# Kernel tuning notes

Measured on AMD Instinct MI355X. Metric: run time of the kernel, lower is better.

The kernel has to match this reference:

```python
import jax, jax.numpy as jnp
import numpy as np
from jax import lax

B, T, V = 128, 256, 64
HF = 32   # MLP feature-imputation hidden
CTX = 32  # context hidden
HID = 64  # LSTM hidden


def _uniform(k, shape, fan):
    s = 1.0 / np.sqrt(fan)
    return jax.random.uniform(k, shape, jnp.float32, -s, s)


def setup_inputs():
    key = jax.random.key(0)
    ks = jax.random.split(key, 40)
    values = jax.random.normal(ks[0], (B, T, V), jnp.float32)
    masks = (jax.random.uniform(ks[1], (B, T, V)) > 0.3).astype(jnp.float32)
    deltas = jax.random.uniform(ks[2], (B, T, V), jnp.float32) * 5.0
    lengths = jax.random.randint(ks[3], (B,), T // 2, T + 1)
    min_vals = jnp.min(values, axis=1, keepdims=True)
    max_vals = jnp.max(values, axis=1, keepdims=True)
    D_in = 2 * V + 2 * CTX
    return dict(
        lengths=lengths, values=values, masks=masks, deltas=deltas,
        min_vals=min_vals, max_vals=max_vals,
        W_decay=_uniform(ks[4], (V, V), V), b_decay=_uniform(ks[5], (V,), V),
        W_feat=_uniform(ks[6], (V, HF, V), V), b_feat=_uniform(ks[7], (V, HF), V),
        W_nl1=_uniform(ks[8], (HF, HF), HF), b_nl1=_uniform(ks[9], (HF,), HF),
        W_nl2=_uniform(ks[10], (1, HF), HF), b_nl2=_uniform(ks[11], (1,), HF),
        Wc1=_uniform(ks[12], (2 * CTX, 3 * V + 1), 3 * V + 1), bc1=_uniform(ks[13], (2 * CTX,), 3 * V + 1),
        Wc2=_uniform(ks[14], (CTX, 2 * CTX), 2 * CTX), bc2=_uniform(ks[15], (CTX,), 2 * CTX),
        W_ih_g=_uniform(ks[16], (3 * CTX, 2 * V), CTX), W_hh_g=_uniform(ks[17], (3 * CTX, CTX), CTX),
        b_ih_g=_uniform(ks[18], (3 * CTX,), CTX), b_hh_g=_uniform(ks[19], (3 * CTX,), CTX),
        W_init=_uniform(ks[20], (2 * HID, 2 * CTX), 2 * CTX), b_init=_uniform(ks[21], (2 * HID,), 2 * CTX),
        W_ih_f=_uniform(ks[22], (4 * HID, D_in), HID), W_hh_f=_uniform(ks[23], (4 * HID, HID), HID),
        b_ih_f=_uniform(ks[24], (4 * HID,), HID), b_hh_f=_uniform(ks[25], (4 * HID,), HID),
        W_ih_b=_uniform(ks[26], (4 * HID, D_in), HID), W_hh_b=_uniform(ks[27], (4 * HID, HID), HID),
        b_ih_b=_uniform(ks[28], (4 * HID,), HID), b_hh_b=_uniform(ks[29], (4 * HID,), HID),
        W_ri=_uniform(ks[30], (V, 2 * HID), 2 * HID), b_ri=_uniform(ks[31], (V,), 2 * HID),
        W_fu=_uniform(ks[32], (V, 2 * V), 2 * V), b_fu=_uniform(ks[33], (V,), 2 * V),
    )


def _gru(x, h, Wih, Whh, bih, bhh):
    gi = x @ Wih.T + bih
    gh = h @ Whh.T + bhh
    ir, iz, inn = jnp.split(gi, 3, axis=-1)
    hr, hz, hn = jnp.split(gh, 3, axis=-1)
    r = jax.nn.sigmoid(ir + hr)
    z = jax.nn.sigmoid(iz + hz)
    n = jnp.tanh(inn + r * hn)
    return (1.0 - z) * n + z * h


def _lstm(x, h, c, Wih, Whh, bih, bhh):
    g = x @ Wih.T + bih + h @ Whh.T + bhh
    i, f, gg, o = jnp.split(g, 4, axis=-1)
    c = jax.nn.sigmoid(f) * c + jax.nn.sigmoid(i) * jnp.tanh(gg)
    h = jax.nn.sigmoid(o) * jnp.tanh(c)
    return h, c


def _forward(lengths, values, masks, deltas, min_vals, max_vals,
             W_decay, b_decay, W_feat, b_feat, W_nl1, b_nl1, W_nl2, b_nl2,
             Wc1, bc1, Wc2, bc2, W_ih_g, W_hh_g, b_ih_g, b_hh_g,
             W_init, b_init, W_ih_f, W_hh_f, b_ih_f, b_hh_f,
             W_ih_b, W_hh_b, b_ih_b, b_hh_b, W_ri, b_ri, W_fu, b_fu):
    Bb, Tt, Vv = values.shape
    lf = lengths.astype(jnp.float32)
    pad = (jnp.arange(Tt)[None, :] + 1 <= lengths[:, None]).astype(jnp.float32)  # [B,T]

    msum = masks.sum(axis=1)                       # [B,V] observation counts
    means = values.sum(axis=1) / msum
    var = ((values - means[:, None, :]) ** 2).sum(axis=1) / (msum - 1.0)
    stdev = jnp.sqrt(var)
    missing = 1.0 - msum / lf[:, None]
    stats = jnp.concatenate([lf[:, None], means, stdev, missing], axis=1)  # [B,3V+1]

    mmn = jnp.maximum(max_vals - min_vals, 1e-8)   # [B,1,V]
    nv = (values - min_vals) / mmn
    nmeans = (means - min_vals[:, 0, :]) / mmn[:, 0, :]

    # last-observation-carried-forward x_prime
    nv_tm = jnp.swapaxes(nv, 0, 1)   # [T,B,V]
    m_tm = jnp.swapaxes(masks, 0, 1)

    def pstep(xp, xm):
        x_prev, m_prev = xm
        xp = m_prev * x_prev + (1.0 - m_prev) * xp
        return xp, xp
    _, xp_rest = lax.scan(pstep, nv_tm[0], (nv_tm[:-1], m_tm[:-1]))
    x_prime = jnp.swapaxes(jnp.concatenate([nv_tm[:1], xp_rest], axis=0), 0, 1)

    # InputTemporalDecay: F.linear(d, W*I, b) == d * diag(W) + b
    gamma = jnp.exp(-jax.nn.relu(deltas * jnp.diag(W_decay) + b_decay))
    x_decay = gamma * x_prime + (1.0 - gamma) * nmeans[:, None, :]
    x_complete = masks * nv + (1.0 - masks) * x_decay

    # context vectors
    ctx_mlp = jax.nn.relu(stats @ Wc1.T + bc1) @ Wc2.T + bc2  # [B,CTX]
    x_rnn_tm = jnp.swapaxes(jnp.concatenate([x_complete, masks], axis=-1), 0, 1)  # [T,B,2V]
    pad_tm = jnp.swapaxes(pad, 0, 1)[:, :, None]
    h0 = jnp.zeros((Bb, W_hh_g.shape[1]), values.dtype)

    def gstep(carry, inp):
        h, hn = carry
        x_t, p_t = inp
        h = _gru(x_t, h, W_ih_g, W_hh_g, b_ih_g, b_hh_g)
        hn = p_t * h + (1.0 - p_t) * hn
        return (h, hn), None
    (_, ctx_rnn), _ = lax.scan(gstep, (h0, h0), (x_rnn_tm, pad_tm))
    context = jnp.concatenate([ctx_mlp, ctx_rnn], axis=1)  # [B,2*CTX]

    hinit = context @ W_init.T + b_init  # [B,2H]
    cinit = jnp.tanh(hinit)
    Hh = hinit.shape[1] // 2
    hf0, hb0 = hinit[:, :Hh], hinit[:, Hh:]
    cf0, cb0 = cinit[:, :Hh], cinit[:, Hh:]

    ctx_bt = jnp.broadcast_to(context[:, None, :], (Bb, Tt, context.shape[1]))
    rnn_in_tm = jnp.swapaxes(jnp.concatenate([x_complete, masks, ctx_bt], axis=-1), 0, 1)  # [T,B,D]

    def fstep(carry, x):
        h, c = _lstm(x, carry[0], carry[1], W_ih_f, W_hh_f, b_ih_f, b_hh_f)
        return (h, c), h
    _, hf_rest = lax.scan(fstep, (hf0, cf0), rnn_in_tm[:-1])
    hf_all = jnp.concatenate([hf0[None], hf_rest], axis=0)  # [T,B,H]

    def bstep(carry, x):
        h, c = _lstm(x, carry[0], carry[1], W_ih_b, W_hh_b, b_ih_b, b_hh_b)
        return (h, c), h
    _, hb_rest = lax.scan(bstep, (hb0, cb0), rnn_in_tm[1:][::-1])  # t = T-1 .. 1
    hb_all = jnp.concatenate([hb0[None], hb_rest], axis=0)[::-1]   # time-aligned

    h_cat = jnp.concatenate([hf_all, hb_all], axis=-1)  # [T,B,2H]
    rnn_imp = jnp.swapaxes(h_cat @ W_ri.T + b_ri, 0, 1)  # [B,T,V]

    # per-variable masked feature imputation (no self-connection)
    eye = jnp.eye(Vv, dtype=values.dtype)
    Wm = W_feat * (1.0 - eye[:, None, :])                 # [V,HF,V]
    hidden = jnp.einsum('btv,ghv->btgh', x_complete, Wm) + b_feat  # [B,T,V,HF]
    z = jax.nn.relu(hidden) @ W_nl1.T + b_nl1
    feat_imp = (jax.nn.relu(z) @ W_nl2.T + b_nl2)[..., 0]  # [B,T,V]

    beta = jax.nn.sigmoid(jnp.concatenate([gamma, masks], axis=-1) @ W_fu.T + b_fu)
    final_imp = beta * feat_imp + (1.0 - beta) * rnn_imp

    # unnormalize all three estimates; stack as [3,B,T,V]
    out = jnp.stack([rnn_imp, feat_imp, final_imp], axis=0) * mmn[None] + min_vals[None]
    return out


def reference(lengths, values, masks, deltas, min_vals, max_vals,
              W_decay, b_decay, W_feat, b_feat, W_nl1, b_nl1, W_nl2, b_nl2,
              Wc1, bc1, Wc2, bc2, W_ih_g, W_hh_g, b_ih_g, b_hh_g,
              W_init, b_init, W_ih_f, W_hh_f, b_ih_f, b_hh_f,
              W_ih_b, W_hh_b, b_ih_b, b_hh_b, W_ri, b_ri, W_fu, b_fu):
    return _forward(lengths, values, masks, deltas, min_vals, max_vals,
                    W_decay, b_decay, W_feat, b_feat, W_nl1, b_nl1, W_nl2, b_nl2,
                    Wc1, bc1, Wc2, bc2, W_ih_g, W_hh_g, b_ih_g, b_hh_g,
                    W_init, b_init, W_ih_f, W_hh_f, b_ih_f, b_hh_f,
                    W_ih_b, W_hh_b, b_ih_b, b_hh_b, W_ri, b_ri, W_fu, b_fu)
```

## Files before the change

### kernel.cpp

```cpp
#include <hip/hip_runtime.h>
#include <hip/hip_fp16.h>

static constexpr int NB = 128;
static constexpr int NT = 256;
static constexpr int NV = 64;
static constexpr int NBT = NB * NT;
static constexpr int NBTV = NBT * NV;

typedef __attribute__((ext_vector_type(8))) short short8;
typedef __attribute__((ext_vector_type(4))) float f32x4;
typedef __attribute__((ext_vector_type(4))) float fvec4;

__device__ __forceinline__ void wave_lds_fence() {
    __builtin_amdgcn_sched_barrier(0);
    asm volatile("s_waitcnt lgkmcnt(0)" ::: "memory");
    __builtin_amdgcn_sched_barrier(0);
}

__device__ __forceinline__ void block_sync_lds() {
    __builtin_amdgcn_sched_barrier(0);
    asm volatile("s_waitcnt lgkmcnt(0)" ::: "memory");
    __builtin_amdgcn_s_barrier();
    asm volatile("" ::: "memory");
    __builtin_amdgcn_sched_barrier(0);
}

__device__ __forceinline__ unsigned short f2bf(float x) {
    unsigned int u = __float_as_uint(x);
    return (unsigned short)((u + 0x7FFFu + ((u >> 16) & 1u)) >> 16);
}
__device__ __forceinline__ float bf2f(unsigned short b) {
    return __uint_as_float(((unsigned int)b) << 16);
}
__device__ __forceinline__ unsigned short f2h(float x) {
    union { _Float16 h; unsigned short u; } c; c.h = (_Float16)x; return c.u;
}
__device__ __forceinline__ float fsigm(float x) {
    return __builtin_amdgcn_rcpf(1.0f + __expf(-x));
}
__device__ __forceinline__ float ftanh(float x) {
    return 1.0f - 2.0f * __builtin_amdgcn_rcpf(1.0f + __expf(2.0f * x));
}

__device__ __forceinline__ short8 pack8(float4 a, float4 b) {
    short8 r;
    r[0] = (short)f2bf(a.x); r[1] = (short)f2bf(a.y); r[2] = (short)f2bf(a.z); r[3] = (short)f2bf(a.w);
    r[4] = (short)f2bf(b.x); r[5] = (short)f2bf(b.y); r[6] = (short)f2bf(b.z); r[7] = (short)f2bf(b.w);
    return r;
}

__device__ __forceinline__ void dot4(float4& acc, const float4 wv, const float4 xv) {
    acc.x = fmaf(wv.x, xv.x, acc.x);
    acc.y = fmaf(wv.y, xv.y, acc.y);
    acc.z = fmaf(wv.z, xv.z, acc.z);
    acc.w = fmaf(wv.w, xv.w, acc.w);
}

__global__ __launch_bounds__(256) void k_prep(
    const float* __restrict__ Wf, const float* __restrict__ Wihf,
    const float* __restrict__ Wihb, const float* __restrict__ Wihg,
    const float* __restrict__ Whhf, const float* __restrict__ Whhb,
    const float* __restrict__ Whhg, const float* __restrict__ Wri,
    const float* __restrict__ Wfu,
    unsigned short* __restrict__ wbf, float* __restrict__ wdiag,
    unsigned short* __restrict__ wgf, unsigned short* __restrict__ wgb,
    unsigned short* __restrict__ wgg,
    unsigned short* __restrict__ whhf_h, unsigned short* __restrict__ whhb_h,
    unsigned short* __restrict__ whhg_h,
    unsigned short* __restrict__ wri_bf, unsigned short* __restrict__ wfu_bf) {
    int i = blockIdx.x * 256 + threadIdx.x;
    if (i < NV * 32 * NV) wbf[i] = f2bf(Wf[i]);
    if (i < 2048) wdiag[i] = bf2f(f2bf(Wf[i * 64 + (i >> 5)]));
    if (i < 32768) {
        int n = i >> 7, k = i & 127;
        wgf[i] = f2bf(Wihf[n * 192 + k]);
        wgb[i] = f2bf(Wihb[n * 192 + k]);
    }
    if (i < 12288) wgg[i] = f2bf(Wihg[i]);
    if (i < 16384) { whhf_h[i] = f2h(Whhf[i]); whhb_h[i] = f2h(Whhb[i]); }
    if (i < 3072) whhg_h[i] = f2h(Whhg[i]);
    if (i < 8192) { wri_bf[i] = f2bf(Wri[i]); wfu_bf[i] = f2bf(Wfu[i]); }
}

__global__ __launch_bounds__(256) void k_fill(
    const int* __restrict__ lengths,
    const float* __restrict__ values, const float* __restrict__ masks,
    const float* __restrict__ deltas, const float* __restrict__ minv,
    const float* __restrict__ maxv,
    const float* __restrict__ Wd, const float* __restrict__ bd,
    float* __restrict__ stats,
    float* __restrict__ mmn_ws, float* __restrict__ nmeans_ws,
    float* __restrict__ xcomp, float* __restrict__ gam) {
    int b = blockIdx.x; int tid = threadIdx.x;
    int v = tid & 63; int tc = tid >> 6;
    float mn = minv[b * NV + v];
    size_t base = (size_t)b * NT * NV + v;
    __shared__ float red[3][4][64];
    __shared__ float lastv[4][64];
    __shared__ int hasf[4][64];
    __shared__ float nv0s[64];
    __shared__ float smm[64], snm[64];
    int t0 = tc * 64;
    float sv = 0.f, sq = 0.f, sm = 0.f;
    float last = 0.f; int has = 0;
    for (int t = t0; t < t0 + 64; t++) {
        float val = values[base + (size_t)t * NV];
        float m = masks[base + (size_t)t * NV];
        sv += val; sq += val * val; sm += m;
        if (m != 0.f) { last = val; has = 1; }
        if (tc == 0 && t == 0) nv0s[v] = val;
    }
    red[0][tc][v] = sv; red[1][tc][v] = sq; red[2][tc][v] = sm;
    lastv[tc][v] = last; hasf[tc][v] = has;
    __syncthreads();
    if (tc == 0) {
        sv = red[0][0][v] + red[0][1][v] + red[0][2][v] + red[0][3][v];
        sq = red[1][0][v] + red[1][1][v] + red[1][2][v] + red[1][3][v];
        sm = red[2][0][v] + red[2][1][v] + red[2][2][v] + red[2][3][v];
        float mean = sv / sm;
        float var = (sq - 2.0f * mean * sv + (float)NT * mean * mean) / (sm - 1.0f);
        var = fmaxf(var, 0.0f);
        float sd = sqrtf(var);
        float lf = (float)lengths[b];
        float miss = 1.0f - sm / lf;
        float mx = maxv[b * NV + v];
        float mm = fmaxf(mx - mn, 1e-8f);
        float* st = stats + b * 256;
        if (v == 0) st[0] = lf;
        st[1 + v] = mean; st[65 + v] = sd; st[129 + v] = miss;
        float nmean = (mean - mn) / mm;
        mmn_ws[b * NV + v] = mm;
        nmeans_ws[b * NV + v] = nmean;
        smm[v] = mm; snm[v] = nmean;
    }
    __syncthreads();
    float mm = smm[v];
    float nmean = snm[v];
    float wd = Wd[v * NV + v], bdv = bd[v];
    float xp = (nv0s[v] - mn) / mm;
    for (int q = tc - 1; q >= 0; q--) {
        if (hasf[q][v]) { xp = (lastv[q][v] - mn) / mm; break; }
    }
    for (int t = t0; t < t0 + 64; t++) {
        size_t i = base + (size_t)t * NV;
        float val = values[i], m = masks[i], d = deltas[i];
        float nv = (val - mn) / mm;
        float g = expf(-fmaxf(fmaf(d, wd, bdv), 0.0f));
        float xd = g * xp + (1.0f - g) * nmean;
        float xc = m * nv + (1.0f - m) * xd;
        xcomp[i] = xc; gam[i] = g;
        xp = (m != 0.f) ? nv : xp;
    }
}

__global__ __launch_bounds__(256) void k_gates_g(
    const float* __restrict__ xcomp, const float* __restrict__ masks,
    const unsigned short* __restrict__ wgg, const float* __restrict__ bihg,
    float* __restrict__ gg) {
    int wave = threadIdx.x >> 6, lane = threadIdx.x & 63;
    int bt0 = blockIdx.x * 64 + wave * 16;
    int r = lane & 15, kc = lane >> 4;
    const float* xr = xcomp + (size_t)(bt0 + r) * NV + kc * 8;
    const float* mr = masks + (size_t)(bt0 + r) * NV + kc * 8;
    short8 af0 = pack8(*(const float4*)(xr), *(const float4*)(xr + 4));
    short8 af1 = pack8(*(const float4*)(xr + 32), *(const float4*)(xr + 36));
    short8 af2 = pack8(*(const float4*)(mr), *(const float4*)(mr + 4));
    short8 af3 = pack8(*(const float4*)(mr + 32), *(const float4*)(mr + 36));
    #pragma unroll 3
    for (int nt = 0; nt < 6; nt++) {
        const unsigned short* w = wgg + (size_t)(nt * 16 + r) * 128 + kc * 8;
        float bias = bihg[nt * 16 + r];
        f32x4 acc = {bias, bias, bias, bias};
        acc = __builtin_amdgcn_mfma_f32_16x16x32_bf16(af0, *(const short8*)(w), acc, 0, 0, 0);
        acc = __builtin_amdgcn_mfma_f32_16x16x32_bf16(af1, *(const short8*)(w + 32), acc, 0, 0, 0);
        acc = __builtin_amdgcn_mfma_f32_16x16x32_bf16(af2, *(const short8*)(w + 64), acc, 0, 0, 0);
        acc = __builtin_amdgcn_mfma_f32_16x16x32_bf16(af3, *(const short8*)(w + 96), acc, 0, 0, 0);
        #pragma unroll
        for (int i = 0; i < 4; i++)
            gg[(size_t)(bt0 + kc * 4 + i) * 96 + nt * 16 + r] = acc[i];
    }
}

#define GRU_STEP(T, GIN) { \
    const int t_ = (T); const int p_ = t_ & 1; \
    int4 raw_[4]; \
    const int4* hp_ = (const int4*)hsg[g][s]; \
    _Pragma("unroll") for (int q = 0; q < 4; q++) raw_[q] = hp_[q]; \
    const __half2* hhv_ = (const __half2*)raw_; \
    __half2 a0_ = zh2, a1_ = zh2, a2_ = zh2, a3_ = zh2; \
    _Pragma("unroll") for (int q = 0; q < 16; q += 4) { \
        a0_ = __hfma2(w2[q],     hhv_[q],     a0_); \
        a1_ = __hfma2(w2[q + 1], hhv_[q + 1], a1_); \
        a2_ = __hfma2(w2[q + 2], hhv_[q + 2], a2_); \
        a3_ = __hfma2(w2[q + 3], hhv_[q + 3], a3_); } \
    __half2 sA_ = __hadd2(__hadd2(a0_, a1_), __hadd2(a2_, a3_)); \
    float d_ = __low2float(sA_) + __high2float(sA_); \
    if (g < 2) { \
        gexg[p_][s][n][g] = GIN + bh + d_; \
    } else { \
        gexg[p_][s][n][2] = bh + d_; \
        gexg[p_][s][n][3] = GIN; \
    } \
    block_sync_lds(); \
    float qx_ = gexg[p_][s][n][0], qy_ = gexg[p_][s][n][1]; \
    float qz_ = gexg[p_][s][n][2], qw_ = gexg[p_][s][n][3]; \
    float rr_ = fsigm(qx_); \
    float zz_ = fsigm(qy_); \
    float nn_ = ftanh(qw_ + rr_ * qz_); \
    float h_ = (1.f - zz_) * nn_ + zz_ * hprev; \
    hprev = h_; \
    if (t_ < len) hn = h_; \
    hsg[g][s][n] = f2h(h_); \
    wave_lds_fence(); \
}

#define FEAT_BODY(BT0) { \
    int bt0 = (BT0); \
    int r = lane & 15, kc = lane >> 4; \
    unsigned short* hbw = hbs[wave]; \
    float* lx = ldsx[wave]; \
    float* flw = fls[wave]; \
    short8 a0, a1; \
    { \
        const float* xr = xcomp + (size_t)(bt0 + r) * NV + kc * 8; \
        a0 = pack8(*(const float4*)(xr), *(const float4*)(xr + 4)); \
        a1 = pack8(*(const float4*)(xr + 32), *(const float4*)(xr + 36)); \
    } \
    { \
        int gc0 = kc * 16; \
        const float* xr2 = xcomp + (size_t)(bt0 + r) * NV + gc0; \
        _Pragma("unroll") for (int e = 0; e < 16; e += 4) { \
            float4 p = *(const float4*)(xr2 + e); \
            lx[(gc0 + e + 0) * 16 + r] = bf2f(f2bf(p.x)); \
            lx[(gc0 + e + 1) * 16 + r] = bf2f(f2bf(p.y)); \
            lx[(gc0 + e + 2) * 16 + r] = bf2f(f2bf(p.z)); \
            lx[(gc0 + e + 3) * 16 + r] = bf2f(f2bf(p.w)); \
        } \
    } \
    short8 wb0, wb1; \
    { \
        const float* w = Wnl1 + r * 32 + kc * 8; \
        wb0 = pack8(*(const float4*)w, *(const float4*)(w + 4)); \
        const float* w2p = Wnl1 + (16 + r) * 32 + kc * 8; \
        wb1 = pack8(*(const float4*)w2p, *(const float4*)(w2p + 4)); \
    } \
    float b0i[4], b1i[4], w2a[4], w2b[4]; \
    _Pragma("unroll") for (int i = 0; i < 4; i++) { \
        b0i[i] = bnl1[kc * 4 + i]; \
        b1i[i] = bnl1[16 + kc * 4 + i]; \
        w2a[i] = Wnl2[kc * 4 + i]; \
        w2b[i] = Wnl2[16 + kc * 4 + i]; \
    } \
    float bn2 = bnl2[0]; \
    __builtin_amdgcn_wave_barrier(); \
    _Pragma("unroll 2") for (int g = 0; g < 64; g++) { \
        __builtin_amdgcn_wave_barrier(); \
        float xv[4]; \
        _Pragma("unroll") for (int i = 0; i < 4; i++) xv[i] = lx[g * 16 + kc * 4 + i]; \
        _Pragma("unroll") for (int f = 0; f < 2; f++) { \
            int n0 = g * 32 + f * 16; \
            const unsigned short* wrow = wbf + (size_t)(n0 + r) * 64; \
            short8 b0 = *(const short8*)(wrow + kc * 8); \
            short8 b1 = *(const short8*)(wrow + 32 + kc * 8); \
            f32x4 acc = {0.f, 0.f, 0.f, 0.f}; \
            acc = __builtin_amdgcn_mfma_f32_16x16x32_bf16(a0, b0, acc, 0, 0, 0); \
            acc = __builtin_amdgcn_mfma_f32_16x16x32_bf16(a1, b1, acc, 0, 0, 0); \
            int n = n0 + r; \
            float wd = wdiag[n], bs = bfeat[n]; \
            _Pragma("unroll") for (int i = 0; i < 4; i++) { \
                float h = acc[i] - xv[i] * wd + bs; \
                h = fmaxf(h, 0.0f); \
                hbw[(kc * 4 + i) * 32 + f * 16 + r] = f2bf(h); \
            } \
        } \
        __builtin_amdgcn_wave_barrier(); \
        short8 ah = *(const short8*)(hbw + r * 32 + kc * 8); \
        f32x4 zt0 = {0.f, 0.f, 0.f, 0.f}, zt1 = {0.f, 0.f, 0.f, 0.f}; \
        zt0 = __builtin_amdgcn_mfma_f32_16x16x32_bf16(wb0, ah, zt0, 0, 0, 0); \
        zt1 = __builtin_amdgcn_mfma_f32_16x16x32_bf16(wb1, ah, zt1, 0, 0, 0); \
        float p = 0.f; \
        _Pragma("unroll") for (int i = 0; i < 4; i++) { \
            p = fmaf(fmaxf(zt0[i] + b0i[i], 0.0f), w2a[i], p); \
            p = fmaf(fmaxf(zt1[i] + b1i[i], 0.0f), w2b[i], p); \
        } \
        p += __shfl_xor(p, 16, 64); \
        p += __shfl_xor(p, 32, 64); \
        if (lane < 16) flw[lane * 65 + g] = p + bn2; \
    } \
    __builtin_amdgcn_wave_barrier(); \
    _Pragma("unroll") for (int q = 0; q < 16; q++) \
        feat_out[(size_t)(bt0 + q) * NV + lane] = flw[q * 65 + lane]; \
}

__global__ __launch_bounds__(256, 1) void k_mid(
    const float* __restrict__ gg_t, const int* __restrict__ lengths,
    const unsigned short* __restrict__ whhg_h, const float* __restrict__ bhh,
    float* __restrict__ ctx,
    const float* __restrict__ stats, const float* __restrict__ Wc1,
    const float* __restrict__ bc1, const float* __restrict__ Wc2,
    const float* __restrict__ bc2,
    const float* __restrict__ xcomp, const float* __restrict__ masks,
    const unsigned short* __restrict__ wgf, const unsigned short* __restrict__ wgb,
    float* __restrict__ gf, float* __restrict__ gb) {
    __shared__ __align__(16) unsigned short hsg[3][2][32];
    __shared__ __align__(16) float gexg[2][2][32][5];
    __shared__ __align__(16) float ss[193];
    __shared__ float h1[64];

    int bx = blockIdx.x;
    int tid = threadIdx.x;

    if (bx < 64) {
        int b0 = bx * 2;
        int g = tid >> 6;
        int lane = tid & 63;
        int s = lane >> 5, n = lane & 31;
        if (g == 3) {
            for (int t = 0; t < NT; t++) block_sync_lds();
            return;
        }
        int b = b0 + s;
        const __half2 zh2 = __float2half2_rn(0.f);
        int4 w4[4];
        {
            const int4* wp = (const int4*)(whhg_h + (size_t)(g * 32 + n) * 32);
            #pragma unroll
            for (int q = 0; q < 4; q++) w4[q] = wp[q];
        }
        const __half2* w2 = (const __half2*)w4;
        float bh = bhh[g * 32 + n];
        int len = lengths[b];
        float hprev = 0.f, hn = 0.f;
        hsg[g][s][n] = f2h(0.f);
        const float* gbase = gg_t + (size_t)b * NT * 96;
        #define GGIDX(T) ((size_t)(T) * 96 + g * 32 + n)
        float gi0 = gbase[GGIDX(0)];
        float gi1 = gbase[GGIDX(1)];
        float gi2 = gbase[GGIDX(2)];
        float gi3 = gbase[GGIDX(3)];
        wave_lds_fence();
        for (int t = 0; t < 252; t += 4) {
            GRU_STEP(t, gi0)
            gi0 = gbase[GGIDX(t + 4)];
            GRU_STEP(t + 1, gi1)
            gi1 = gbase[GGIDX(t + 5)];
            GRU_STEP(t + 2, gi2)
            gi2 = gbase[GGIDX(t + 6)];
            GRU_STEP(t + 3, gi3)
            gi3 = gbase[GGIDX(t + 7)];
        }
        GRU_STEP(252, gi0)
        GRU_STEP(253, gi1)
        GRU_STEP(254, gi2)
        GRU_STEP(255, gi3)
        #undef GGIDX
        if (g == 0) ctx[(b0 + s) * 64 + 32 + n] = hn;
    } else if (bx < 192) {
        if (tid >= 64) return;
        int b = bx - 64;
        ss[tid] = stats[b * 256 + tid];
        ss[64 + tid] = stats[b * 256 + 64 + tid];
        ss[128 + tid] = stats[b * 256 + 128 + tid];
        if (tid == 0) ss[192] = stats[b * 256 + 192];
        wave_lds_fence();
        float acc = bc1[tid];
        const float* w = Wc1 + (size_t)tid * 193;
        for (int k = 0; k < 193; k++) acc = fmaf(w[k], ss[k], acc);
        h1[tid] = fmaxf(acc, 0.f);
        wave_lds_fence();
        if (tid < 32) {
            float a = bc2[tid];
            const float* w2 = Wc2 + tid * 64;
            for (int k = 0; k < 64; k++) a = fmaf(w2[k], h1[k], a);
            ctx[b * 64 + tid] = a;
        }
    } else {
        int wave = tid >> 6, lane = tid & 63;
        int bt0 = (bx - 192) * 64 + wave * 16;
        int r = lane & 15, kc = lane >> 4;
        const float* xr = xcomp + (size_t)(bt0 + r) * NV + kc * 8;
        const float* mr = masks + (size_t)(bt0 + r) * NV + kc * 8;
        short8 af0 = pack8(*(const float4*)(xr), *(const float4*)(xr + 4));
        short8 af1 = pack8(*(const float4*)(xr + 32), *(const float4*)(xr + 36));
        short8 af2 = pack8(*(const float4*)(mr), *(const float4*)(mr + 4));
        short8 af3 = pack8(*(const float4*)(mr + 32), *(const float4*)(mr + 36));
        #pragma unroll 4
        for (int nt = 0; nt < 16; nt++) {
            const unsigned short* w = wgf + (size_t)(nt * 16 + r) * 128 + kc * 8;
            f32x4 acc = {0.f, 0.f, 0.f, 0.f};
            acc = __builtin_amdgcn_mfma_f32_16x16x32_bf16(af0, *(const short8*)(w), acc, 0, 0, 0);
            acc = __builtin_amdgcn_mfma_f32_16x16x32_bf16(af1, *(const short8*)(w + 32), acc, 0, 0, 0);
            acc = __builtin_amdgcn_mfma_f32_16x16x32_bf16(af2, *(const short8*)(w + 64), acc, 0, 0, 0);
            acc = __builtin_amdgcn_mfma_f32_16x16x32_bf16(af3, *(const short8*)(w + 96), acc, 0, 0, 0);
            int col = nt * 16 + r, g = col >> 6, n = col & 63;
            #pragma unroll
            for (int i = 0; i < 4; i++)
                gf[((size_t)(bt0 + kc * 4 + i) * 64 + n) * 4 + g] = acc[i];
        }
        #pragma unroll 4
        for (int nt = 0; nt < 16; nt++) {
            const unsigned short* w = wgb + (size_t)(nt * 16 + r) * 128 + kc * 8;
            f32x4 acc = {0.f, 0.f, 0.f, 0.f};
            acc = __builtin_amdgcn_mfma_f32_16x16x32_bf16(af0, *(const short8*)(w), acc, 0, 0, 0);
            acc = __builtin_amdgcn_mfma_f32_16x16x32_bf16(af1, *(const short8*)(w + 32), acc, 0, 0, 0);
            acc = __builtin_amdgcn_mfma_f32_16x16x32_bf16(af2, *(const short8*)(w + 64), acc, 0, 0, 0);
            acc = __builtin_amdgcn_mfma_f32_16x16x32_bf16(af3, *(const short8*)(w + 96), acc, 0, 0, 0);
            int col = nt * 16 + r, g = col >> 6, n = col & 63;
            #pragma unroll
            for (int i = 0; i < 4; i++)
                gb[((size_t)(bt0 + kc * 4 + i) * 64 + n) * 4 + g] = acc[i];
        }
    }
}

#define LSTM_STEP(S, GIN) { \
    const int s_ = (S); const int p_ = s_ & 1; \
    int4 raw_[8]; \
    const int4* hp_ = (const int4*)hs[g]; \
    _Pragma("unroll") for (int q = 0; q < 8; q++) raw_[q] = hp_[q]; \
    const __half2* hhv_ = (const __half2*)raw_; \
    __half2 a0_ = zh2, a1_ = zh2, a2_ = zh2, a3_ = zh2; \
    _Pragma("unroll") for (int q = 0; q < 32; q += 4) { \
        a0_ = __hfma2(w2[q],     hhv_[q],     a0_); \
        a1_ = __hfma2(w2[q + 1], hhv_[q + 1], a1_); \
        a2_ = __hfma2(w2[q + 2], hhv_[q + 2], a2_); \
        a3_ = __hfma2(w2[q + 3], hhv_[q + 3], a3_); } \
    __half2 sA_ = __hadd2(__hadd2(a0_, a1_), __hadd2(a2_, a3_)); \
    float d_ = __low2float(sA_) + __high2float(sA_); \
    gex[p_][n][g] = GIN + ctg + d_; \
    block_sync_lds(); \
    float qx_ = gex[p_][n][0], qy_ = gex[p_][n][1]; \
    float qz_ = gex[p_][n][2], qw_ = gex[p_][n][3]; \
    float ii_ = fsigm(qx_); \
    float ff_ = fsigm(qy_); \
    float gv_ = ftanh(qz_); \
    float oo_ = fsigm(qw_); \
    c = ff_ * c + ii_ * gv_; \
    float hv_ = oo_ * ftanh(c); \
    if (g == 0) { \
        int tout_ = dir ? (NT - 2 - s_) : (s_ + 1); \
        hall[((size_t)b * NT + tout_) * NV + n] = hv_; \
    } \
    hs[g][n] = f2h(hv_); \
    wave_lds_fence(); \
}

__global__ __launch_bounds__(256, 1) void k_lstm(
    const float* __restrict__ gf, const float* __restrict__ gb,
    const float* __restrict__ ctx,
    const unsigned short* __restrict__ whhf_h, const unsigned short* __restrict__ whhb_h,
    const float* __restrict__ Wihf, const float* __restrict__ Wihb,
    const float* __restrict__ bihf, const float* __restrict__ bhhf,
    const float* __restrict__ bihb, const float* __restrict__ bhhb,
    const float* __restrict__ Wini, const float* __restrict__ bini,
    float* __restrict__ out0, float* __restrict__ out1,
    const float* __restrict__ xcomp, const unsigned short* __restrict__ wbf,
    const float* __restrict__ wdiag, const float* __restrict__ bfeat,
    const float* __restrict__ Wnl1, const float* __restrict__ bnl1,
    const float* __restrict__ Wnl2, const float* __restrict__ bnl2,
    float* __restrict__ feat_out) {
    __shared__ __align__(16) unsigned short hs[4][64];
    __shared__ __align__(16) float gex[2][64][5];
    __shared__ __align__(16) float sctx[64];
    __shared__ __align__(16) float sh0[64];
    __shared__ __align__(16) unsigned short hbs[4][16 * 32];
    __shared__ __align__(16) float ldsx[4][64 * 16];
    __shared__ __align__(16) float fls[4][16 * 65];

    int bx = blockIdx.x;
    int tid = threadIdx.x;

    if (bx >= 256) {
        int wave = tid >> 6; int lane = tid & 63;
        FEAT_BODY((bx - 256) * 64 + wave * 16)
        return;
    }

    int dir = bx >> 7; int b = bx & 127;
    int g = tid >> 6;
    int n = tid & 63;
    const float* gates = dir ? gb : gf;
    const unsigned short* wsrc = dir ? whhb_h : whhf_h;
    float* hall = dir ? out1 : out0;
    const __half2 zh2 = __float2half2_rn(0.f);
    int4 w4[8];
    {
        const int4* wp = (const int4*)(wsrc + (size_t)(g * 64 + n) * 64);
        #pragma unroll
        for (int q = 0; q < 8; q++) w4[q] = wp[q];
    }
    const __half2* w2 = (const __half2*)w4;
    size_t gbase = (size_t)b * NT * 256;
    #define GIDX(S) (gbase + (size_t)(dir ? (NT - 1 - (S)) : (S)) * 256 + n * 4 + g)
    float gi0 = gates[GIDX(0)];
    float gi1 = gates[GIDX(1)];
    float gi2 = gates[GIDX(2)];
    float gi3 = gates[GIDX(3)];
    if (tid < 64) sctx[tid] = ctx[b * 64 + tid];
    __syncthreads();
    float ctg;
    {
        const float4* wc = (const float4*)((dir ? Wihb : Wihf) + (size_t)tid * 192 + 128);
        float bias = dir ? (bihb[tid] + bhhb[tid]) : (bihf[tid] + bhhf[tid]);
        const float4* c4 = (const float4*)sctx;
        float4 a = {0, 0, 0, 0};
        #pragma unroll
        for (int q = 0; q < 16; q++) dot4(a, wc[q], c4[q]);
        ctg = bias + a.x + a.y + a.z + a.w;
    }
    if (tid < 64) {
        const float4* wi = (const float4*)(Wini + (size_t)(dir * 64 + tid) * 64);
        const float4* c4 = (const float4*)sctx;
        float4 a = {0, 0, 0, 0};
        #pragma unroll
        for (int q = 0; q < 16; q++) dot4(a, wi[q], c4[q]);
        sh0[tid] = bini[dir * 64 + tid] + a.x + a.y + a.z + a.w;
    }
    __syncthreads();
    float c;
    {
        float h0 = sh0[n];
        c = ftanh(h0);
        hs[g][n] = f2h(h0);
        if (g == 0) {
            int t0 = dir ? (NT - 1) : 0;
            hall[((size_t)b * NT + t0) * NV + n] = h0;
        }
    }
    wave_lds_fence();
    for (int sx = 0; sx < 252; sx += 4) {
        LSTM_STEP(sx, gi0)
        gi0 = gates[GIDX(sx + 4)];
        LSTM_STEP(sx + 1, gi1)
        gi1 = gates[GIDX(sx + 5)];
        LSTM_STEP(sx + 2, gi2)
        gi2 = gates[GIDX(sx + 6)];
        LSTM_STEP(sx + 3, gi3)
        gi3 = gates[GIDX(sx + 7)];
    }
    LSTM_STEP(252, gi0)
    LSTM_STEP(253, gi1)
    LSTM_STEP(254, gi2)
    #undef GIDX
}

__global__ __launch_bounds__(256) void k_post(
    const float* __restrict__ gam, const float* __restrict__ masks,
    const unsigned short* __restrict__ wri_bf, const unsigned short* __restrict__ wfu_bf,
    const float* __restrict__ bri, const float* __restrict__ bfu,
    const float* __restrict__ mmn_ws, const float* __restrict__ minv,
    float* out0, float* out1, float* out2) {
    int wave = threadIdx.x >> 6, lane = threadIdx.x & 63;
    int bt0 = blockIdx.x * 64 + wave * 16;
    int r = lane & 15, kc = lane >> 4;
    int b = bt0 >> 8;
    const float* h0r = out0 + (size_t)(bt0 + r) * NV + kc * 8;
    const float* h1r = out1 + (size_t)(bt0 + r) * NV + kc * 8;
    const float* gr  = gam  + (size_t)(bt0 + r) * NV + kc * 8;
    const float* mr  = masks + (size_t)(bt0 + r) * NV + kc * 8;
    short8 A0 = pack8(*(const float4*)(h0r), *(const float4*)(h0r + 4));
    short8 A1 = pack8(*(const float4*)(h0r + 32), *(const float4*)(h0r + 36));
    short8 A2 = pack8(*(const float4*)(h1r), *(const float4*)(h1r + 4));
    short8 A3 = pack8(*(const float4*)(h1r + 32), *(const float4*)(h1r + 36));
    short8 G0 = pack8(*(const float4*)(gr), *(const float4*)(gr + 4));
    short8 G1 = pack8(*(const float4*)(gr + 32), *(const float4*)(gr + 36));
    short8 M0 = pack8(*(const float4*)(mr), *(const float4*)(mr + 4));
    short8 M1 = pack8(*(const float4*)(mr + 32), *(const float4*)(mr + 36));
    #pragma unroll
    for (int nt = 0; nt < 4; nt++) {
        int n = nt * 16 + r;
        const unsigned short* wr = wri_bf + (size_t)n * 128 + kc * 8;
        const unsigned short* wf = wfu_bf + (size_t)n * 128 + kc * 8;
        float bi = bri[n], bf_ = bfu[n];
        f32x4 racc = {bi, bi, bi, bi};
        f32x4 bacc = {bf_, bf_, bf_, bf_};
        racc = __builtin_amdgcn_mfma_f32_16x16x32_bf16(A0, *(const short8*)(wr), racc, 0, 0, 0);
        racc = __builtin_amdgcn_mfma_f32_16x16x32_bf16(A1, *(const short8*)(wr + 32), racc, 0, 0, 0);
        racc = __builtin_amdgcn_mfma_f32_16x16x32_bf16(A2, *(const short8*)(wr + 64), racc, 0, 0, 0);
        racc = __builtin_amdgcn_mfma_f32_16x16x32_bf16(A3, *(const short8*)(wr + 96), racc, 0, 0, 0);
        bacc = __builtin_amdgcn_mfma_f32_16x16x32_bf16(G0, *(const short8*)(wf), bacc, 0, 0, 0);
        bacc = __builtin_amdgcn_mfma_f32_16x16x32_bf16(G1, *(const short8*)(wf + 32), bacc, 0, 0, 0);
        bacc = __builtin_amdgcn_mfma_f32_16x16x32_bf16(M0, *(const short8*)(wf + 64), bacc, 0, 0, 0);
        bacc = __builtin_amdgcn_mfma_f32_16x16x32_bf16(M1, *(const short8*)(wf + 96), bacc, 0, 0, 0);
        float mm = mmn_ws[b * NV + n], mn = minv[b * NV + n];
        #pragma unroll
        for (int i = 0; i < 4; i++) {
            int row = bt0 + kc * 4 + i;
            size_t idx = (size_t)row * NV + n;
            float rn = racc[i];
            float beta = fsigm(bacc[i]);
            float ft = out2[idx];
            float fin = beta * ft + (1.0f - beta) * rn;
            out0[idx] = fmaf(rn, mm, mn);
            out1[idx] = fmaf(ft, mm, mn);
            out2[idx] = fmaf(fin, mm, mn);
        }
    }
}

extern "C" void kernel_launch(void* const* d_in, const int* in_sizes, int n_in,
                              void* d_out, int out_size, void* d_ws, size_t ws_size,
                              hipStream_t stream) {
    const int*   lengths  = (const int*)d_in[0];
    const float* values   = (const float*)d_in[1];
    const float* masks    = (const float*)d_in[2];
    const float* deltas   = (const float*)d_in[3];
    const float* min_vals = (const float*)d_in[4];
    const float* max_vals = (const float*)d_in[5];
    const float* W_decay  = (const float*)d_in[6];
    const float* b_decay  = (const float*)d_in[7];
    const float* W_feat   = (const float*)d_in[8];
    const float* b_feat   = (const float*)d_in[9];
    const float* W_nl1    = (const float*)d_in[10];
    const float* b_nl1    = (const float*)d_in[11];
    const float* W_nl2    = (const float*)d_in[12];
    const float* b_nl2    = (const float*)d_in[13];
    const float* Wc1      = (const float*)d_in[14];
    const float* bc1      = (const float*)d_in[15];
    const float* Wc2      = (const float*)d_in[16];
    const float* bc2      = (const float*)d_in[17];
    const float* W_ih_g   = (const float*)d_in[18];
    const float* W_hh_g   = (const float*)d_in[19];
    const float* b_ih_g   = (const float*)d_in[20];
    const float* b_hh_g   = (const float*)d_in[21];
    const float* W_init   = (const float*)d_in[22];
    const float* b_init   = (const float*)d_in[23];
    const float* W_ih_f   = (const float*)d_in[24];
    const float* W_hh_f   = (const float*)d_in[25];
    const float* b_ih_f   = (const float*)d_in[26];
    const float* b_hh_f   = (const float*)d_in[27];
    const float* W_ih_b   = (const float*)d_in[28];
    const float* W_hh_b   = (const float*)d_in[29];
    const float* b_ih_b   = (const float*)d_in[30];
    const float* b_hh_b   = (const float*)d_in[31];
    const float* W_ri     = (const float*)d_in[32];
    const float* b_ri     = (const float*)d_in[33];
    const float* W_fu     = (const float*)d_in[34];
    const float* b_fu     = (const float*)d_in[35];

    float* ws = (float*)d_ws;
    float* xcomp  = ws;
    float* gam    = ws + 2097152;
    unsigned short* wri_bf = (unsigned short*)(ws + 4194304);
    unsigned short* wfu_bf = (unsigned short*)(ws + 4198400);
    float* stats  = ws + 6291456;
    float* mmn    = ws + 6324224;
    float* nmeans = ws + 6332416;
    float* ctx    = ws + 6340608;
    unsigned short* wbf = (unsigned short*)(ws + 6365184);
    float* wdiag  = ws + 6430720;
    unsigned short* wgf = (unsigned short*)(ws + 6432768);
    unsigned short* wgb = (unsigned short*)(ws + 6449152);
    unsigned short* wgg = (unsigned short*)(ws + 6465536);
    unsigned short* whhf_h = (unsigned short*)(ws + 6471680);
    unsigned short* whhb_h = (unsigned short*)(ws + 6479872);
    unsigned short* whhg_h = (unsigned short*)(ws + 6488064);
    float* gates_f = ws + 6555136;
    float* gates_b = ws + 14943744;
    float* gates_g = ws + 23332352;

    float* out0 = (float*)d_out;
    float* out1 = out0 + NBTV;
    float* out2 = out0 + 2 * NBTV;

    k_prep<<<512, 256, 0, stream>>>(W_feat, W_ih_f, W_ih_b, W_ih_g, W_hh_f, W_hh_b, W_hh_g,
                                    W_ri, W_fu,
                                    wbf, wdiag, wgf, wgb, wgg, whhf_h, whhb_h, whhg_h,
                                    wri_bf, wfu_bf);
    k_fill<<<NB, 256, 0, stream>>>(lengths, values, masks, deltas, min_vals, max_vals,
                                   W_decay, b_decay, stats, mmn, nmeans, xcomp, gam);
    k_gates_g<<<NBT / 64, 256, 0, stream>>>(xcomp, masks, wgg, b_ih_g, gates_g);
    k_mid<<<704, 256, 0, stream>>>(gates_g, lengths, whhg_h, b_hh_g, ctx,
                                   stats, Wc1, bc1, Wc2, bc2,
                                   xcomp, masks, wgf, wgb, gates_f, gates_b);
    k_lstm<<<768, 256, 0, stream>>>(gates_f, gates_b, ctx, whhf_h, whhb_h,
                                    W_ih_f, W_ih_b, b_ih_f, b_hh_f, b_ih_b, b_hh_b,
                                    W_init, b_init, out0, out1,
                                    xcomp, wbf, wdiag, b_feat, W_nl1, b_nl1, W_nl2, b_nl2, out2);
    k_post<<<NBT / 64, 256, 0, stream>>>(gam, masks, wri_bf, wfu_bf, b_ri, b_fu, mmn, min_vals,
                                         out0, out1, out2);
}
```

Before: 295.0 us.

## Fuse GRU input gates into fill kernel and rebalance feature/beta work across kernels

Removes the separate k_gates_g launch by computing the GRU input-gate GEMM inside k_fill, reading the bf16 xcomp from shared memory instead of reloading it from global. Half of the feature-imputation MLP blocks move from k_lstm into k_mid so they run alongside the context GRU. The beta (fusion gate) GEMM moves into spare k_lstm blocks and is stored as fp16 in the gates_g buffer, which is no longer needed at that point, so k_post only does the residual GEMM. The aim is to fill idle CUs during the latency-bound recurrent kernels and cut launches and global traffic. The costs are 32KB of extra LDS in k_fill, only 128 blocks doing the gate GEMM, and beta rounded to fp16.

```diff
diff --git a/kernel.cpp b/kernel.cpp
--- a/kernel.cpp
+++ b/kernel.cpp
@@ -34,6 +34,9 @@
 }
 __device__ __forceinline__ unsigned short f2h(float x) {
     union { _Float16 h; unsigned short u; } c; c.h = (_Float16)x; return c.u;
+}
+__device__ __forceinline__ float h2f(unsigned short u) {
+    union { unsigned short u; _Float16 h; } c; c.u = u; return (float)c.h;
 }
 __device__ __forceinline__ float fsigm(float x) {
     return __builtin_amdgcn_rcpf(1.0f + __expf(-x));
@@ -90,7 +93,9 @@
     const float* __restrict__ Wd, const float* __restrict__ bd,
     float* __restrict__ stats,
     float* __restrict__ mmn_ws, float* __restrict__ nmeans_ws,
-    float* __restrict__ xcomp, float* __restrict__ gam) {
+    float* __restrict__ xcomp, float* __restrict__ gam,
+    const unsigned short* __restrict__ wgg, const float* __restrict__ bihg,
+    float* __restrict__ gg) {
     int b = blockIdx.x; int tid = threadIdx.x;
     int v = tid & 63; int tc = tid >> 6;
     float mn = minv[b * NV + v];
@@ -100,6 +105,7 @@
     __shared__ int hasf[4][64];
     __shared__ float nv0s[64];
     __shared__ float smm[64], snm[64];
+    __shared__ __align__(16) unsigned short sxc[256][64];
     int t0 = tc * 64;
     float sv = 0.f, sq = 0.f, sm = 0.f;
     float last = 0.f; int has = 0;
@@ -149,35 +155,33 @@
         float xd = g * xp + (1.0f - g) * nmean;
         float xc = m * nv + (1.0f - m) * xd;
         xcomp[i] = xc; gam[i] = g;
+        sxc[t][v] = f2bf(xc);
         xp = (m != 0.f) ? nv : xp;
     }
-}
-
-__global__ __launch_bounds__(256) void k_gates_g(
-    const float* __restrict__ xcomp, const float* __restrict__ masks,
-    const unsigned short* __restrict__ wgg, const float* __restrict__ bihg,
-    float* __restrict__ gg) {
-    int wave = threadIdx.x >> 6, lane = threadIdx.x & 63;
-    int bt0 = blockIdx.x * 64 + wave * 16;
+    __syncthreads();
+    int lane = tid & 63;
     int r = lane & 15, kc = lane >> 4;
-    const float* xr = xcomp + (size_t)(bt0 + r) * NV + kc * 8;
-    const float* mr = masks + (size_t)(bt0 + r) * NV + kc * 8;
-    short8 af0 = pack8(*(const float4*)(xr), *(const float4*)(xr + 4));
-    short8 af1 = pack8(*(const float4*)(xr + 32), *(const float4*)(xr + 36));
-    short8 af2 = pack8(*(const float4*)(mr), *(const float4*)(mr + 4));
-    short8 af3 = pack8(*(const float4*)(mr + 32), *(const float4*)(mr + 36));
-    #pragma unroll 3
-    for (int nt = 0; nt < 6; nt++) {
-        const unsigned short* w = wgg + (size_t)(nt * 16 + r) * 128 + kc * 8;
-        float bias = bihg[nt * 16 + r];
-        f32x4 acc = {bias, bias, bias, bias};
-        acc = __builtin_amdgcn_mfma_f32_16x16x32_bf16(af0, *(const short8*)(w), acc, 0, 0, 0);
-        acc = __builtin_amdgcn_mfma_f32_16x16x32_bf16(af1, *(const short8*)(w + 32), acc, 0, 0, 0);
-        acc = __builtin_amdgcn_mfma_f32_16x16x32_bf16(af2, *(const short8*)(w + 64), acc, 0, 0, 0);
-        acc = __builtin_amdgcn_mfma_f32_16x16x32_bf16(af3, *(const short8*)(w + 96), acc, 0, 0, 0);
-        #pragma unroll
-        for (int i = 0; i < 4; i++)
-            gg[(size_t)(bt0 + kc * 4 + i) * 96 + nt * 16 + r] = acc[i];
+    for (int tile = 0; tile < 4; tile++) {
+        int trow = (tc * 4 + tile) * 16;
+        int bt0 = b * NT + trow;
+        short8 af0 = *(const short8*)&sxc[trow + r][kc * 8];
+        short8 af1 = *(const short8*)&sxc[trow + r][32 + kc * 8];
+        const float* mr = masks + ((size_t)bt0 + r) * NV + kc * 8;
+        short8 af2 = pack8(*(const float4*)(mr), *(const float4*)(mr + 4));
+        short8 af3 = pack8(*(const float4*)(mr + 32), *(const float4*)(mr + 36));
+        #pragma unroll 3
+        for (int nt = 0; nt < 6; nt++) {
+            const unsigned short* w = wgg + (size_t)(nt * 16 + r) * 128 + kc * 8;
+            float bias = bihg[nt * 16 + r];
+            f32x4 acc = {bias, bias, bias, bias};
+            acc = __builtin_amdgcn_mfma_f32_16x16x32_bf16(af0, *(const short8*)(w), acc, 0, 0, 0);
+            acc = __builtin_amdgcn_mfma_f32_16x16x32_bf16(af1, *(const short8*)(w + 32), acc, 0, 0, 0);
+            acc = __builtin_amdgcn_mfma_f32_16x16x32_bf16(af2, *(const short8*)(w + 64), acc, 0, 0, 0);
+            acc = __builtin_amdgcn_mfma_f32_16x16x32_bf16(af3, *(const short8*)(w + 96), acc, 0, 0, 0);
+            #pragma unroll
+            for (int i = 0; i < 4; i++)
+                gg[(size_t)(bt0 + kc * 4 + i) * 96 + nt * 16 + r] = acc[i];
+        }
     }
 }
 
@@ -300,12 +304,20 @@
     const float* __restrict__ bc1, const float* __restrict__ Wc2,
     const float* __restrict__ bc2,
     const float* __restrict__ xcomp, const float* __restrict__ masks,
+    const unsigned short* __restrict__ wbf,
+    const float* __restrict__ wdiag, const float* __restrict__ bfeat,
+    const float* __restrict__ Wnl1, const float* __restrict__ bnl1,
+    const float* __restrict__ Wnl2, const float* __restrict__ bnl2,
+    float* __restrict__ feat_out,
     const unsigned short* __restrict__ wgf, const unsigned short* __restrict__ wgb,
     float* __restrict__ gf, float* __restrict__ gb) {
     __shared__ __align__(16) unsigned short hsg[3][2][32];
     __shared__ __align__(16) float gexg[2][2][32][5];
     __shared__ __align__(16) float ss[193];
     __shared__ float h1[64];
+    __shared__ __align__(16) unsigned short hbs[4][16 * 32];
+    __shared__ __align__(16) float ldsx[4][64 * 16];
+    __shared__ __align__(16) float fls[4][16 * 65];
 
     int bx = blockIdx.x;
     int tid = threadIdx.x;
@@ -374,9 +386,12 @@
             for (int k = 0; k < 64; k++) a = fmaf(w2[k], h1[k], a);
             ctx[b * 64 + tid] = a;
         }
+    } else if (bx < 448) {
+        int wave = tid >> 6; int lane = tid & 63;
+        FEAT_BODY((bx - 192) * 64 + wave * 16)
     } else {
         int wave = tid >> 6, lane = tid & 63;
-        int bt0 = (bx - 192) * 64 + wave * 16;
+        int bt0 = (bx - 448) * 64 + wave * 16;
         int r = lane & 15, kc = lane >> 4;
         const float* xr = xcomp + (size_t)(bt0 + r) * NV + kc * 8;
         const float* mr = masks + (size_t)(bt0 + r) * NV + kc * 8;
@@ -458,7 +473,10 @@
     const float* __restrict__ wdiag, const float* __restrict__ bfeat,
     const float* __restrict__ Wnl1, const float* __restrict__ bnl1,
     const float* __restrict__ Wnl2, const float* __restrict__ bnl2,
-    float* __restrict__ feat_out) {
+    float* __restrict__ feat_out,
+    const float* __restrict__ gam, const float* __restrict__ masks,
+    const unsigned short* __restrict__ wfu_bf, const float* __restrict__ bfu,
+    unsigned short* __restrict__ bet) {
     __shared__ __align__(16) unsigned short hs[4][64];
     __shared__ __align__(16) float gex[2][64][5];
     __shared__ __align__(16) float sctx[64];
@@ -470,9 +488,38 @@
     int bx = blockIdx.x;
     int tid = threadIdx.x;
 
+    if (bx >= 512) {
+        int wave = tid >> 6, lane = tid & 63;
+        int r = lane & 15, kc = lane >> 4;
+        #pragma unroll
+        for (int tile = 0; tile < 4; tile++) {
+            int bt0 = (bx - 512) * 256 + (wave * 4 + tile) * 16;
+            const float* gr = gam + (size_t)(bt0 + r) * NV + kc * 8;
+            const float* mr = masks + (size_t)(bt0 + r) * NV + kc * 8;
+            short8 G0 = pack8(*(const float4*)(gr), *(const float4*)(gr + 4));
+            short8 G1 = pack8(*(const float4*)(gr + 32), *(const float4*)(gr + 36));
+            short8 M0 = pack8(*(const float4*)(mr), *(const float4*)(mr + 4));
+            short8 M1 = pack8(*(const float4*)(mr + 32), *(const float4*)(mr + 36));
+            #pragma unroll
+            for (int nt = 0; nt < 4; nt++) {
+                int n = nt * 16 + r;
+                const unsigned short* wf = wfu_bf + (size_t)n * 128 + kc * 8;
+                float bf_ = bfu[n];
+                f32x4 bacc = {bf_, bf_, bf_, bf_};
+                bacc = __builtin_amdgcn_mfma_f32_16x16x32_bf16(G0, *(const short8*)(wf), bacc, 0, 0, 0);
+                bacc = __builtin_amdgcn_mfma_f32_16x16x32_bf16(G1, *(const short8*)(wf + 32), bacc, 0, 0, 0);
+                bacc = __builtin_amdgcn_mfma_f32_16x16x32_bf16(M0, *(const short8*)(wf + 64), bacc, 0, 0, 0);
+                bacc = __builtin_amdgcn_mfma_f32_16x16x32_bf16(M1, *(const short8*)(wf + 96), bacc, 0, 0, 0);
+                #pragma unroll
+                for (int i = 0; i < 4; i++)
+                    bet[(size_t)(bt0 + kc * 4 + i) * 64 + n] = f2h(fsigm(bacc[i]));
+            }
+        }
+        return;
+    }
     if (bx >= 256) {
         int wave = tid >> 6; int lane = tid & 63;
-        FEAT_BODY((bx - 256) * 64 + wave * 16)
+        FEAT_BODY((bx - 256) * 64 + 16384 + wave * 16)
         return;
     }
 
@@ -545,9 +592,9 @@
 }
 
 __global__ __launch_bounds__(256) void k_post(
-    const float* __restrict__ gam, const float* __restrict__ masks,
-    const unsigned short* __restrict__ wri_bf, const unsigned short* __restrict__ wfu_bf,
-    const float* __restrict__ bri, const float* __restrict__ bfu,
+    const unsigned short* __restrict__ bet,
+    const unsigned short* __restrict__ wri_bf,
+    const float* __restrict__ bri,
     const float* __restrict__ mmn_ws, const float* __restrict__ minv,
     float* out0, float* out1, float* out2) {
     int wave = threadIdx.x >> 6, lane = threadIdx.x & 63;
@@ -556,39 +603,27 @@
     int b = bt0 >> 8;
     const float* h0r = out0 + (size_t)(bt0 + r) * NV + kc * 8;
     const float* h1r = out1 + (size_t)(bt0 + r) * NV + kc * 8;
-    const float* gr  = gam  + (size_t)(bt0 + r) * NV + kc * 8;
-    const float* mr  = masks + (size_t)(bt0 + r) * NV + kc * 8;
     short8 A0 = pack8(*(const float4*)(h0r), *(const float4*)(h0r + 4));
     short8 A1 = pack8(*(const float4*)(h0r + 32), *(const float4*)(h0r + 36));
     short8 A2 = pack8(*(const float4*)(h1r), *(const float4*)(h1r + 4));
     short8 A3 = pack8(*(const float4*)(h1r + 32), *(const float4*)(h1r + 36));
-    short8 G0 = pack8(*(const float4*)(gr), *(const float4*)(gr + 4));
-    short8 G1 = pack8(*(const float4*)(gr + 32), *(const float4*)(gr + 36));
-    short8 M0 = pack8(*(const float4*)(mr), *(const float4*)(mr + 4));
-    short8 M1 = pack8(*(const float4*)(mr + 32), *(const float4*)(mr + 36));
     #pragma unroll
     for (int nt = 0; nt < 4; nt++) {
         int n = nt * 16 + r;
         const unsigned short* wr = wri_bf + (size_t)n * 128 + kc * 8;
-        const unsigned short* wf = wfu_bf + (size_t)n * 128 + kc * 8;
-        float bi = bri[n], bf_ = bfu[n];
+        float bi = bri[n];
         f32x4 racc = {bi, bi, bi, bi};
-        f32x4 bacc = {bf_, bf_, bf_, bf_};
         racc = __builtin_amdgcn_mfma_f32_16x16x32_bf16(A0, *(const short8*)(wr), racc, 0, 0, 0);
         racc = __builtin_amdgcn_mfma_f32_16x16x32_bf16(A1, *(const short8*)(wr + 32), racc, 0, 0, 0);
         racc = __builtin_amdgcn_mfma_f32_16x16x32_bf16(A2, *(const short8*)(wr + 64), racc, 0, 0, 0);
         racc = __builtin_amdgcn_mfma_f32_16x16x32_bf16(A3, *(const short8*)(wr + 96), racc, 0, 0, 0);
-        bacc = __builtin_amdgcn_mfma_f32_16x16x32_bf16(G0, *(const short8*)(wf), bacc, 0, 0, 0);
-        bacc = __builtin_amdgcn_mfma_f32_16x16x32_bf16(G1, *(const short8*)(wf + 32), bacc, 0, 0, 0);
-        bacc = __builtin_amdgcn_mfma_f32_16x16x32_bf16(M0, *(const short8*)(wf + 64), bacc, 0, 0, 0);
-        bacc = __builtin_amdgcn_mfma_f32_16x16x32_bf16(M1, *(const short8*)(wf + 96), bacc, 0, 0, 0);
         float mm = mmn_ws[b * NV + n], mn = minv[b * NV + n];
         #pragma unroll
         for (int i = 0; i < 4; i++) {
             int row = bt0 + kc * 4 + i;
             size_t idx = (size_t)row * NV + n;
             float rn = racc[i];
-            float beta = fsigm(bacc[i]);
+            float beta = h2f(bet[idx]);
             float ft = out2[idx];
             float fin = beta * ft + (1.0f - beta) * rn;
             out0[idx] = fmaf(rn, mm, mn);
@@ -658,6 +693,7 @@
     float* gates_f = ws + 6555136;
     float* gates_b = ws + 14943744;
     float* gates_g = ws + 23332352;
+    unsigned short* bet = (unsigned short*)gates_g;
 
     float* out0 = (float*)d_out;
     float* out1 = out0 + NBTV;
@@ -668,15 +704,16 @@
                                     wbf, wdiag, wgf, wgb, wgg, whhf_h, whhb_h, whhg_h,
                                     wri_bf, wfu_bf);
     k_fill<<<NB, 256, 0, stream>>>(lengths, values, masks, deltas, min_vals, max_vals,
-                                   W_decay, b_decay, stats, mmn, nmeans, xcomp, gam);
-    k_gates_g<<<NBT / 64, 256, 0, stream>>>(xcomp, masks, wgg, b_ih_g, gates_g);
-    k_mid<<<704, 256, 0, stream>>>(gates_g, lengths, whhg_h, b_hh_g, ctx,
+                                   W_decay, b_decay, stats, mmn, nmeans, xcomp, gam,
+                                   wgg, b_ih_g, gates_g);
+    k_mid<<<960, 256, 0, stream>>>(gates_g, lengths, whhg_h, b_hh_g, ctx,
                                    stats, Wc1, bc1, Wc2, bc2,
-                                   xcomp, masks, wgf, wgb, gates_f, gates_b);
-    k_lstm<<<768, 256, 0, stream>>>(gates_f, gates_b, ctx, whhf_h, whhb_h,
+                                   xcomp, masks, wbf, wdiag, b_feat, W_nl1, b_nl1, W_nl2, b_nl2, out2,
+                                   wgf, wgb, gates_f, gates_b);
+    k_lstm<<<640, 256, 0, stream>>>(gates_f, gates_b, ctx, whhf_h, whhb_h,
                                     W_ih_f, W_ih_b, b_ih_f, b_hh_f, b_ih_b, b_hh_b,
                                     W_init, b_init, out0, out1,
-                                    xcomp, wbf, wdiag, b_feat, W_nl1, b_nl1, W_nl2, b_nl2, out2);
-    k_post<<<NBT / 64, 256, 0, stream>>>(gam, masks, wri_bf, wfu_bf, b_ri, b_fu, mmn, min_vals,
-                                         out0, out1, out2);
-}
+                                    xcomp, wbf, wdiag, b_feat, W_nl1, b_nl1, W_nl2, b_nl2, out2,
+                                    gam, masks, wfu_bf, b_fu, bet);
+    k_post<<<NBT / 64, 256, 0, stream>>>(bet, wri_bf, b_ri, mmn, min_vals, out0, out1, out2);
+}
```

New measurement: 334.7 us. 1.13x slower.
